# Performance work log

Measured on AMD Instinct MI355X. Metric: run time of the kernel, lower is better.

Reference implementation:

```python
import jax, jax.numpy as jnp
import numpy as np

HIDDEN_DIM = 2048
NUM_HEADS = 16
HEAD_DIM = HIDDEN_DIM // NUM_HEADS
BATCH = 2
SEQ = 2048


def setup_inputs() -> dict:
    key = jax.random.key(0)
    ks = jax.random.split(key, 5)
    scale = 1.0 / np.sqrt(HIDDEN_DIM)
    x = jax.random.normal(ks[0], (BATCH, SEQ, HIDDEN_DIM), dtype=jnp.float32)
    w_q = jax.random.normal(ks[1], (HIDDEN_DIM, HIDDEN_DIM), dtype=jnp.float32) * scale
    w_k = jax.random.normal(ks[2], (HIDDEN_DIM, HIDDEN_DIM), dtype=jnp.float32) * scale
    w_v = jax.random.normal(ks[3], (HIDDEN_DIM, HIDDEN_DIM), dtype=jnp.float32) * scale
    w_o = jax.random.normal(ks[4], (HIDDEN_DIM, HIDDEN_DIM), dtype=jnp.float32) * scale
    return {"x": x, "w_q": w_q, "w_k": w_k, "w_v": w_v, "w_o": w_o}


def reference(x, w_q, w_k, w_v, w_o):
    # Projections: x @ W.T  (weights stored as (out, in) like torch)
    q = jnp.einsum('bsd,ed->bse', x, w_q)
    k = jnp.einsum('bsd,ed->bse', x, w_k)
    v = jnp.einsum('bsd,ed->bse', x, w_v)
    b, s, _ = q.shape
    # split heads: (b, h, s, hd)
    q = q.reshape(b, s, NUM_HEADS, HEAD_DIM).transpose(0, 2, 1, 3)
    k = k.reshape(b, s, NUM_HEADS, HEAD_DIM).transpose(0, 2, 1, 3)
    v = v.reshape(b, s, NUM_HEADS, HEAD_DIM).transpose(0, 2, 1, 3)
    scale = 1.0 / np.sqrt(HEAD_DIM)
    # Online-softmax tiling in the source (causal=False default) is
    # mathematically identical to standard softmax attention.
    scores = jnp.einsum('bhqd,bhkd->bhqk', q, k) * scale
    p = jax.nn.softmax(scores, axis=-1)
    o = jnp.einsum('bhqk,bhkd->bhqd', p, v)
    o = o.transpose(0, 2, 1, 3).reshape(b, s, HIDDEN_DIM)
    return jnp.einsum('bsd,ed->bse', o, w_o)
```

## Files before the change

kernel.cpp:

```cpp
#include <hip/hip_runtime.h>


typedef _Float16 half8 __attribute__((ext_vector_type(8)));
typedef _Float16 half4 __attribute__((ext_vector_type(4)));
typedef float floatx4 __attribute__((ext_vector_type(4)));

__device__ __forceinline__ void async16(const void* g, void* l) {
  __builtin_amdgcn_global_load_lds((__attribute__((address_space(1))) void*)(g),
                                   (__attribute__((address_space(3))) void*)(l),
                                   16, 0, 0);
}

__global__ void cvt_all(const float* __restrict__ x, const float* __restrict__ w0,
                        const float* __restrict__ w1, const float* __restrict__ w2,
                        const float* __restrict__ w3, _Float16* __restrict__ xh,
                        _Float16* __restrict__ wh, float scale0) {
  int i = blockIdx.x * blockDim.x + threadIdx.x;
  const int XQ = 1 << 21;
  float sc = 1.0f;
  const float* src;
  _Float16* dst;
  int j;
  if (i < XQ) { src = x; dst = xh; j = i; }
  else {
    int t = i - XQ;
    int m = t >> 20;
    src = (m == 0) ? w0 : (m == 1) ? w1 : (m == 2) ? w2 : w3;
    if (m == 0) sc = scale0;
    dst = wh; j = t;
  }
  int js = (i < XQ) ? j : (j & ((1 << 20) - 1));
  float4 v = reinterpret_cast<const float4*>(src)[js];
  union { _Float16 h[4]; short4 s; } u;
  u.h[0] = (_Float16)(v.x * sc); u.h[1] = (_Float16)(v.y * sc);
  u.h[2] = (_Float16)(v.z * sc); u.h[3] = (_Float16)(v.w * sc);
  reinterpret_cast<short4*>(dst)[j] = u.s;
}

__device__ __forceinline__ void rdA4(half8 (&f)[4][2], const _Float16* base,
                                     int ch0, int ch1) {
#pragma unroll
  for (int mt = 0; mt < 4; ++mt) {
    f[mt][0] = *reinterpret_cast<const half8*>(base + mt * 2048 + ch0);
    f[mt][1] = *reinterpret_cast<const half8*>(base + mt * 2048 + ch1);
  }
}
__device__ __forceinline__ void rdB2(half8 (&f)[2][2], const _Float16* base,
                                     int ch0, int ch1) {
#pragma unroll
  for (int nt = 0; nt < 2; ++nt) {
    f[nt][0] = *reinterpret_cast<const half8*>(base + nt * 4096 + ch0);
    f[nt][1] = *reinterpret_cast<const half8*>(base + nt * 4096 + ch1);
  }
}
template <int MO, int NO>
__device__ __forceinline__ void mmg16(floatx4 (&acc)[8][4], const half8 (&af)[4][2],
                                      const half8 (&bf)[2][2]) {
#pragma unroll
  for (int kk = 0; kk < 2; ++kk)
#pragma unroll
    for (int mt = 0; mt < 4; ++mt)
#pragma unroll
      for (int nt = 0; nt < 2; ++nt)
        acc[MO + mt][NO + nt] = __builtin_amdgcn_mfma_f32_16x16x32_f16(
            af[mt][kk], bf[nt][kk], acc[MO + mt][NO + nt], 0, 0, 0);
}

#define STAGE_AH0(buf, kk) { async16(ags + (kk), &(buf)[ldst]); \
                             async16(ags + 131072 + (kk), &(buf)[4096 + ldst]); }
#define STAGE_AH1(buf, kk) { async16(ags + 262144 + (kk), &(buf)[8192 + ldst]); \
                             async16(ags + 393216 + (kk), &(buf)[12288 + ldst]); }
#define STAGE_BH0(buf, kk) { async16(bgs + (kk), &(buf)[ldst]); \
                             async16(bgs + 131072 + (kk), &(buf)[4096 + ldst]); }
#define STAGE_BH1(buf, kk) { async16(bgs + 262144 + (kk), &(buf)[8192 + ldst]); \
                             async16(bgs + 393216 + (kk), &(buf)[12288 + ldst]); }
#define VMW(n) asm volatile("s_waitcnt vmcnt(" #n ")" ::: "memory")
#define SBAR() __builtin_amdgcn_s_barrier()
#define SCHED() __builtin_amdgcn_sched_barrier(0)
#define PRIO1() __builtin_amdgcn_s_setprio(1)
#define PRIO0() __builtin_amdgcn_s_setprio(0)

__global__ __launch_bounds__(512, 2)
void gemm_nt(const _Float16* __restrict__ A, const _Float16* __restrict__ Bw,
             void* __restrict__ Cv, void* __restrict__ Cv2) {
  __shared__ _Float16 As[2][256 * 64];
  __shared__ _Float16 Bs[2][256 * 64];
  const int tid = threadIdx.x;
  const int wave = tid >> 6, lane = tid & 63;
  const int wm = wave >> 2, wn = wave & 3;
  const int l15 = lane & 15, l4 = lane >> 4;

  const int NBN = 24;
  const int nwg = NBN * 16;
  const int swz = (blockIdx.x & 7) * (nwg >> 3) + (blockIdx.x >> 3);
  const int bn = swz % NBN, bm = swz / NBN;

  const int srow = tid >> 3;
  const int g = (tid & 7) ^ (srow & 7);
  const _Float16* ags = A + (size_t)(bm * 256 + srow) * 2048 + g * 8;
  const _Float16* bgs = Bw + (size_t)(bn * 256 + srow) * 2048 + g * 8;
  const int ldst = tid * 8;

  const int arow = wm * 16 + l15;
  const int brow = wn * 16 + l15;
  const int ch0 = (l4 ^ (l15 & 7)) * 8;
  const int ch1 = ((l4 + 4) ^ (l15 & 7)) * 8;

  STAGE_AH0(As[0], 0); STAGE_BH0(Bs[0], 0);
  STAGE_BH1(Bs[0], 0); STAGE_AH1(As[0], 0);
  STAGE_AH0(As[1], 64); STAGE_BH0(Bs[1], 64);
  VMW(4);
  SBAR();

  floatx4 acc[8][4] = {};
  half8 afA[4][2], afB[4][2], bfA[2][2], bfB[2][2];
  rdA4(afA, &As[0][arow * 64], ch0, ch1);
  rdB2(bfA, &Bs[0][brow * 64], ch0, ch1);

#pragma unroll 2
  for (int t = 0; t < 30; ++t) {
    const int c = t & 1, nx = c ^ 1;
    const int k1 = t * 64 + 64, k2 = t * 64 + 128;
    const _Float16* Ac = &As[c][0];
    const _Float16* Bc = &Bs[c][0];

    PRIO1(); mmg16<0, 0>(acc, afA, bfA); PRIO0();
    rdB2(bfB, Bc + brow * 64 + 8192, ch0, ch1);
    STAGE_BH1(Bs[nx], k1);
    SCHED(); VMW(6); SBAR();

    PRIO1(); mmg16<0, 2>(acc, afA, bfB); PRIO0();
    rdA4(afB, Ac + arow * 64 + 8192, ch0, ch1);
    STAGE_AH1(As[nx], k1);
    SCHED(); VMW(6); SBAR();

    PRIO1(); mmg16<4, 0>(acc, afB, bfA); PRIO0();
    STAGE_AH0(As[c], k2);
    SCHED(); VMW(6); SBAR();

    PRIO1(); mmg16<4, 2>(acc, afB, bfB); PRIO0();
    rdA4(afA, &As[nx][arow * 64], ch0, ch1);
    rdB2(bfA, &Bs[nx][brow * 64], ch0, ch1);
    STAGE_BH0(Bs[c], k2);
    SCHED(); VMW(6); SBAR();
  }

  {
    const _Float16* Ac = &As[0][0];
    const _Float16* Bc = &Bs[0][0];
    PRIO1(); mmg16<0, 0>(acc, afA, bfA); PRIO0();
    rdB2(bfB, Bc + brow * 64 + 8192, ch0, ch1);
    STAGE_BH1(Bs[1], 1984);
    SCHED(); VMW(6); SBAR();

    PRIO1(); mmg16<0, 2>(acc, afA, bfB); PRIO0();
    rdA4(afB, Ac + arow * 64 + 8192, ch0, ch1);
    STAGE_AH1(As[1], 1984);
    SCHED(); VMW(6); SBAR();

    PRIO1(); mmg16<4, 0>(acc, afB, bfA); PRIO0();
    SCHED(); VMW(4); SBAR();

    PRIO1(); mmg16<4, 2>(acc, afB, bfB); PRIO0();
    rdA4(afA, &As[1][arow * 64], ch0, ch1);
    rdB2(bfA, &Bs[1][brow * 64], ch0, ch1);
    SCHED(); VMW(2); SBAR();
  }
  {
    const _Float16* Ac = &As[1][0];
    const _Float16* Bc = &Bs[1][0];
    PRIO1(); mmg16<0, 0>(acc, afA, bfA); PRIO0();
    rdB2(bfB, Bc + brow * 64 + 8192, ch0, ch1);
    SCHED(); VMW(0); SBAR();
    PRIO1(); mmg16<0, 2>(acc, afA, bfB); PRIO0();
    rdA4(afB, Ac + arow * 64 + 8192, ch0, ch1);
    mmg16<4, 0>(acc, afB, bfA);
    mmg16<4, 2>(acc, afB, bfB);
  }

  const int cb0 = bn * 256;
  if (cb0 < 4096) {
    _Float16* C = (_Float16*)Cv + (size_t)(cb0 >> 11) * (4096ull * 2048);
#pragma unroll
    for (int mt = 0; mt < 8; ++mt)
#pragma unroll
      for (int nt = 0; nt < 4; ++nt) {
        int r0 = bm * 256 + mt * 32 + wm * 16 + l4 * 4;
        int cg = (cb0 + nt * 64 + wn * 16 + l15) & 2047;
#pragma unroll
        for (int r = 0; r < 4; ++r)
          C[(size_t)(r0 + r) * 2048 + cg] = (_Float16)acc[mt][nt][r];
      }
  } else {
    _Float16* C = (_Float16*)Cv2;
#pragma unroll
    for (int mt = 0; mt < 8; ++mt)
#pragma unroll
      for (int nt = 0; nt < 4; ++nt) {
        int m0 = bm * 256 + mt * 32 + wm * 16 + l4 * 4;
        int d = cb0 + nt * 64 + wn * 16 + l15 - 4096;
        size_t base = (size_t)(m0 >> 11) * (2048ull * 2048) + (size_t)d * 2048 + (m0 & 2047);
        union { _Float16 h[4]; short4 s; } u;
#pragma unroll
        for (int r = 0; r < 4; ++r) u.h[r] = (_Float16)acc[mt][nt][r];
        *reinterpret_cast<short4*>(C + base) = u.s;
      }
  }
}

__global__ __launch_bounds__(256)
void gemm_wo(const _Float16* __restrict__ A, const _Float16* __restrict__ Bw,
             float* __restrict__ C) {
  __shared__ _Float16 As[128 * 64];
  __shared__ _Float16 Bs[128 * 64];
  const int tid = threadIdx.x;
  const int wave = tid >> 6, lane = tid & 63;
  const int wm = wave >> 1, wn = wave & 1;
  const int l15 = lane & 15, l4 = lane >> 4;
  const int bm = blockIdx.y, bn = blockIdx.x;

  floatx4 acc[4][4] = {};

  for (int k0 = 0; k0 < 2048; k0 += 64) {
    __syncthreads();
#pragma unroll
    for (int i = 0; i < 4; ++i) {
      int c = i * 256 + tid;
      int row = c >> 3, cc = c & 7;
      int gg = cc ^ (row & 7);
      async16(A + (size_t)(bm * 128 + row) * 2048 + k0 + gg * 8, &As[c * 8]);
      async16(Bw + (size_t)(bn * 128 + row) * 2048 + k0 + gg * 8, &Bs[c * 8]);
    }
    __syncthreads();
#pragma unroll
    for (int ks = 0; ks < 2; ++ks) {
      half8 af[4], bf[4];
      int ch = (ks * 4 + l4) ^ (l15 & 7);
#pragma unroll
      for (int t = 0; t < 4; ++t) {
        af[t] = *reinterpret_cast<const half8*>(&As[(wm * 64 + t * 16 + l15) * 64 + ch * 8]);
        bf[t] = *reinterpret_cast<const half8*>(&Bs[(wn * 64 + t * 16 + l15) * 64 + ch * 8]);
      }
#pragma unroll
      for (int mt = 0; mt < 4; ++mt)
#pragma unroll
        for (int nt = 0; nt < 4; ++nt)
          acc[mt][nt] = __builtin_amdgcn_mfma_f32_16x16x32_f16(af[mt], bf[nt], acc[mt][nt], 0, 0, 0);
    }
  }

  const int rbase = bm * 128 + wm * 64;
  const int cbase = bn * 128 + wn * 64;
#pragma unroll
  for (int mt = 0; mt < 4; ++mt)
#pragma unroll
    for (int nt = 0; nt < 4; ++nt) {
      int r0 = rbase + mt * 16 + l4 * 4;
      int cg = cbase + nt * 16 + l15;
#pragma unroll
      for (int r = 0; r < 4; ++r)
        C[(size_t)(r0 + r) * 2048 + cg] = acc[mt][nt][r];
    }
}

__global__ __launch_bounds__(256, 2)
void flash_attn(const _Float16* __restrict__ Q, const _Float16* __restrict__ Kg,
                const _Float16* __restrict__ Vt, _Float16* __restrict__ O) {
  __shared__ _Float16 Ks[2][64 * 128];
  __shared__ _Float16 Vs[2][128 * 64];
  __shared__ _Float16 Ps[128 * 64];
  const int tid = threadIdx.x, wave = tid >> 6, lane = tid & 63;
  const int l15 = lane & 15, l4 = lane >> 4;
  const int bh = blockIdx.y, b = bh >> 4, h = bh & 15;
  const int q0 = blockIdx.x * 128;

  const _Float16* Qp = Q + ((size_t)(b * 2048 + q0 + wave * 32)) * 2048 + h * 128;
  const _Float16* Kp = Kg + (size_t)b * 2048 * 2048 + h * 128;
  const _Float16* Vp = Vt + (size_t)b * 2048 * 2048 + (size_t)(h * 128) * 2048;

  const _Float16* ka[4]; const _Float16* va[4];
  int kl[4], vl[4];
#pragma unroll
  for (int i = 0; i < 4; ++i) {
    int c = i * 256 + tid;
    int row = c >> 4, cc = c & 15, gk = cc ^ (row & 15);
    ka[i] = Kp + (size_t)row * 2048 + gk * 8;
    kl[i] = c * 8;
    int rv = c >> 3, cv = c & 7, gv = cv ^ (rv & 7);
    va[i] = Vp + (size_t)rv * 2048 + gv * 8;
    vl[i] = c * 8;
  }

#pragma unroll
  for (int i = 0; i < 4; ++i) async16(ka[i], &Ks[0][kl[i]]);
#pragma unroll
  for (int i = 0; i < 4; ++i) async16(va[i], &Vs[0][vl[i]]);

  half8 qf[2][4];
#pragma unroll
  for (int qt = 0; qt < 2; ++qt)
#pragma unroll
    for (int ks = 0; ks < 4; ++ks)
      qf[qt][ks] = *reinterpret_cast<const half8*>(
          Qp + (size_t)(qt * 16 + l15) * 2048 + ks * 32 + l4 * 8);

  VMW(0);
  SBAR();

  floatx4 oacc[2][8] = {};
  float lsumq[2] = {0.f, 0.f};

  for (int t = 0; t < 32; ++t) {
    const int c = t & 1, nx = c ^ 1;
    if (t < 31) {
      const size_t kofs = (size_t)(t * 64 + 64);
#pragma unroll
      for (int i = 0; i < 4; ++i) async16(ka[i] + kofs * 2048, &Ks[nx][kl[i]]);
#pragma unroll
      for (int i = 0; i < 4; ++i) async16(va[i] + kofs, &Vs[nx][vl[i]]);
    }

    floatx4 sacc[4][2] = {};
#pragma unroll
    for (int ks = 0; ks < 4; ++ks) {
      half8 kf[4];
#pragma unroll
      for (int st = 0; st < 4; ++st) {
        int row = st * 16 + l15;
        int ch = (ks * 4 + l4) ^ l15;
        kf[st] = *reinterpret_cast<const half8*>(&Ks[c][row * 128 + ch * 8]);
      }
#pragma unroll
      for (int st = 0; st < 4; ++st)
#pragma unroll
        for (int qt = 0; qt < 2; ++qt)
          sacc[st][qt] = __builtin_amdgcn_mfma_f32_16x16x32_f16(kf[st], qf[qt][ks], sacc[st][qt], 0, 0, 0);
    }

#pragma unroll
    for (int qt = 0; qt < 2; ++qt)
#pragma unroll
      for (int st = 0; st < 4; ++st) {
        float p0 = exp2f(sacc[st][qt][0]);
        float p1 = exp2f(sacc[st][qt][1]);
        float p2 = exp2f(sacc[st][qt][2]);
        float p3 = exp2f(sacc[st][qt][3]);
        lsumq[qt] += (p0 + p1) + (p2 + p3);
        half4 pv;
        pv[0] = (_Float16)p0; pv[1] = (_Float16)p1;
        pv[2] = (_Float16)p2; pv[3] = (_Float16)p3;
        int ch = (st * 2 + (l4 >> 1)) ^ (l15 & 7);
        *reinterpret_cast<half4*>(
            &Ps[(wave * 32 + qt * 16 + l15) * 64 + ch * 8 + (l4 & 1) * 4]) = pv;
      }

    __builtin_amdgcn_s_waitcnt(0xC07F);

#pragma unroll
    for (int ks2 = 0; ks2 < 2; ++ks2) {
      half8 pf[2];
#pragma unroll
      for (int mt = 0; mt < 2; ++mt)
        pf[mt] = *reinterpret_cast<const half8*>(
            &Ps[(wave * 32 + mt * 16 + l15) * 64 + (((ks2 * 4 + l4) ^ (l15 & 7)) * 8)]);
#pragma unroll
      for (int nt2 = 0; nt2 < 8; ++nt2) {
        int row = nt2 * 16 + l15;
        int ch = (ks2 * 4 + l4) ^ (row & 7);
        half8 vf = *reinterpret_cast<const half8*>(&Vs[c][row * 64 + ch * 8]);
#pragma unroll
        for (int mt = 0; mt < 2; ++mt)
          oacc[mt][nt2] = __builtin_amdgcn_mfma_f32_16x16x32_f16(pf[mt], vf, oacc[mt][nt2], 0, 0, 0);
      }
    }

    if (t < 31) VMW(0);
    SBAR();
  }

#pragma unroll
  for (int qt = 0; qt < 2; ++qt) {
    lsumq[qt] += __shfl_xor(lsumq[qt], 16);
    lsumq[qt] += __shfl_xor(lsumq[qt], 32);
  }

  _Float16* Op = O + ((size_t)(b * 2048 + q0 + wave * 32)) * 2048 + h * 128;
#pragma unroll
  for (int mt = 0; mt < 2; ++mt)
#pragma unroll
    for (int r = 0; r < 4; ++r) {
      float inv = 1.0f / __shfl(lsumq[mt], l4 * 4 + r);
#pragma unroll
      for (int nt2 = 0; nt2 < 8; ++nt2) {
        int row = mt * 16 + l4 * 4 + r;
        int col = nt2 * 16 + l15;
        Op[(size_t)row * 2048 + col] = (_Float16)(oacc[mt][nt2][r] * inv);
      }
    }
}

extern "C" void kernel_launch(void* const* d_in, const int* in_sizes, int n_in,
                              void* d_out, int out_size, void* d_ws, size_t ws_size,
                              hipStream_t stream) {
  const float* x = (const float*)d_in[0];
  const float* wq = (const float*)d_in[1];
  const float* wk = (const float*)d_in[2];
  const float* wv = (const float*)d_in[3];
  const float* wo = (const float*)d_in[4];
  float* out = (float*)d_out;

  const size_t XN = (size_t)4096 * 2048;
  const size_t WN = (size_t)2048 * 2048;
  _Float16* xh = (_Float16*)d_ws;
  _Float16* qh = xh + XN;
  _Float16* vth = xh + 3 * XN;
  _Float16* oh = xh + 4 * XN;
  _Float16* wqh = xh + 5 * XN;

  const float SM_SCALE = 0.08838834764831845f * 1.4426950408889634f;

  cvt_all<<<dim3(24576), 256, 0, stream>>>(x, wq, wk, wv, wo, xh, wqh, SM_SCALE);
  gemm_nt<<<dim3(384), 512, 0, stream>>>(xh, wqh, qh, vth);
  flash_attn<<<dim3(16, 32), 256, 0, stream>>>(qh, qh + XN, vth, oh);
  gemm_wo<<<dim3(16, 32), 256, 0, stream>>>(oh, wqh + 3 * WN, out);
}
```

Baseline: 382.5 us.

## Double-buffer output-projection GEMM loads and raise wave priority around attention MFMAs

The W_o GEMM now keeps two LDS buffers and issues the async global-to-LDS loads for the next K-tile before computing on the current one, replacing the load-then-sync-then-compute loop. Global-memory latency can then overlap with MFMA work, and launch bounds request two blocks per CU. The flash-attention MFMA sections are wrapped in wave priority raises (PRIO1/PRIO0) to favour matrix issue. In exchange the GEMM uses twice the LDS (64KB per block), which may limit occupancy, and the priority hints may have little effect.

```diff
diff --git a/kernel.cpp b/kernel.cpp
--- a/kernel.cpp
+++ b/kernel.cpp
@@ -208,38 +208,52 @@
   }
 }
 
-__global__ __launch_bounds__(256)
+__global__ __launch_bounds__(256, 2)
 void gemm_wo(const _Float16* __restrict__ A, const _Float16* __restrict__ Bw,
              float* __restrict__ C) {
-  __shared__ _Float16 As[128 * 64];
-  __shared__ _Float16 Bs[128 * 64];
+  __shared__ _Float16 As[2][128 * 64];
+  __shared__ _Float16 Bs[2][128 * 64];
   const int tid = threadIdx.x;
   const int wave = tid >> 6, lane = tid & 63;
   const int wm = wave >> 1, wn = wave & 1;
   const int l15 = lane & 15, l4 = lane >> 4;
   const int bm = blockIdx.y, bn = blockIdx.x;
 
+  const _Float16* ag[4]; const _Float16* bg[4]; int sl[4];
+#pragma unroll
+  for (int i = 0; i < 4; ++i) {
+    int c = i * 256 + tid;
+    int row = c >> 3, cc = c & 7, gg = cc ^ (row & 7);
+    ag[i] = A + (size_t)(bm * 128 + row) * 2048 + gg * 8;
+    bg[i] = Bw + (size_t)(bn * 128 + row) * 2048 + gg * 8;
+    sl[i] = c * 8;
+  }
+
+#pragma unroll
+  for (int i = 0; i < 4; ++i) { async16(ag[i], &As[0][sl[i]]); async16(bg[i], &Bs[0][sl[i]]); }
+  VMW(0);
+  SBAR();
+
   floatx4 acc[4][4] = {};
 
-  for (int k0 = 0; k0 < 2048; k0 += 64) {
-    __syncthreads();
-#pragma unroll
-    for (int i = 0; i < 4; ++i) {
-      int c = i * 256 + tid;
-      int row = c >> 3, cc = c & 7;
-      int gg = cc ^ (row & 7);
-      async16(A + (size_t)(bm * 128 + row) * 2048 + k0 + gg * 8, &As[c * 8]);
-      async16(Bw + (size_t)(bn * 128 + row) * 2048 + k0 + gg * 8, &Bs[c * 8]);
-    }
-    __syncthreads();
+  for (int t = 0; t < 32; ++t) {
+    const int c = t & 1, nx = c ^ 1;
+    if (t < 31) {
+      const int kn = t * 64 + 64;
+#pragma unroll
+      for (int i = 0; i < 4; ++i) {
+        async16(ag[i] + kn, &As[nx][sl[i]]);
+        async16(bg[i] + kn, &Bs[nx][sl[i]]);
+      }
+    }
 #pragma unroll
     for (int ks = 0; ks < 2; ++ks) {
       half8 af[4], bf[4];
       int ch = (ks * 4 + l4) ^ (l15 & 7);
 #pragma unroll
-      for (int t = 0; t < 4; ++t) {
-        af[t] = *reinterpret_cast<const half8*>(&As[(wm * 64 + t * 16 + l15) * 64 + ch * 8]);
-        bf[t] = *reinterpret_cast<const half8*>(&Bs[(wn * 64 + t * 16 + l15) * 64 + ch * 8]);
+      for (int tt = 0; tt < 4; ++tt) {
+        af[tt] = *reinterpret_cast<const half8*>(&As[c][(wm * 64 + tt * 16 + l15) * 64 + ch * 8]);
+        bf[tt] = *reinterpret_cast<const half8*>(&Bs[c][(wn * 64 + tt * 16 + l15) * 64 + ch * 8]);
       }
 #pragma unroll
       for (int mt = 0; mt < 4; ++mt)
@@ -247,6 +261,8 @@
         for (int nt = 0; nt < 4; ++nt)
           acc[mt][nt] = __builtin_amdgcn_mfma_f32_16x16x32_f16(af[mt], bf[nt], acc[mt][nt], 0, 0, 0);
     }
+    if (t < 31) VMW(0);
+    SBAR();
   }
 
   const int rbase = bm * 128 + wm * 64;
@@ -330,11 +346,13 @@
         int ch = (ks * 4 + l4) ^ l15;
         kf[st] = *reinterpret_cast<const half8*>(&Ks[c][row * 128 + ch * 8]);
       }
+      PRIO1();
 #pragma unroll
       for (int st = 0; st < 4; ++st)
 #pragma unroll
         for (int qt = 0; qt < 2; ++qt)
           sacc[st][qt] = __builtin_amdgcn_mfma_f32_16x16x32_f16(kf[st], qf[qt][ks], sacc[st][qt], 0, 0, 0);
+      PRIO0();
     }
 
 #pragma unroll
@@ -363,6 +381,7 @@
       for (int mt = 0; mt < 2; ++mt)
         pf[mt] = *reinterpret_cast<const half8*>(
             &Ps[(wave * 32 + mt * 16 + l15) * 64 + (((ks2 * 4 + l4) ^ (l15 & 7)) * 8)]);
+      PRIO1();
 #pragma unroll
       for (int nt2 = 0; nt2 < 8; ++nt2) {
         int row = nt2 * 16 + l15;
@@ -372,6 +391,7 @@
         for (int mt = 0; mt < 2; ++mt)
           oacc[mt][nt2] = __builtin_amdgcn_mfma_f32_16x16x32_f16(pf[mt], vf, oacc[mt][nt2], 0, 0, 0);
       }
+      PRIO0();
     }
 
     if (t < 31) VMW(0);
```

New measurement: 387.5 us. About the same (+1.3%).
